# Performance work log

Measured on AMD Instinct MI355X. Metric: run time of the kernel, lower is better.

The kernel has to match this reference:

```python
import jax, jax.numpy as jnp
import numpy as np

BN_EPS = 1e-5
N_NODES = 100000
N_EDGES = 1600000
IN_DIM = 128
HID = 256   # 2 * out_dim
OUT_DIM = 128


def setup_inputs() -> dict:
    key = jax.random.key(0)
    ks = jax.random.split(key, 8)
    x = jax.random.normal(ks[0], (N_NODES, IN_DIM), dtype=jnp.float32)
    edge_index = jax.random.randint(ks[1], (2, N_EDGES), 0, N_NODES, dtype=jnp.int32)
    # GINConv learned eps (train_eps=True), init 0
    eps = jnp.zeros((), dtype=jnp.float32)
    # MLP: Linear(in, 2*out) -> BN -> ReLU -> Linear(2*out, out)
    s1 = 1.0 / np.sqrt(IN_DIM)
    s2 = 1.0 / np.sqrt(HID)
    W1 = jax.random.uniform(ks[2], (IN_DIM, HID), jnp.float32, -s1, s1)
    b1 = jax.random.uniform(ks[3], (HID,), jnp.float32, -s1, s1)
    g1 = jnp.ones((HID,), jnp.float32)
    beta1 = jnp.zeros((HID,), jnp.float32)
    W2 = jax.random.uniform(ks[4], (HID, OUT_DIM), jnp.float32, -s2, s2)
    b2 = jax.random.uniform(ks[5], (OUT_DIM,), jnp.float32, -s2, s2)
    # outer BatchNorm
    g2 = jnp.ones((OUT_DIM,), jnp.float32)
    beta2 = jnp.zeros((OUT_DIM,), jnp.float32)
    return {"x": x, "edge_index": edge_index, "eps": eps,
            "W1": W1, "b1": b1, "g1": g1, "beta1": beta1,
            "W2": W2, "b2": b2, "g2": g2, "beta2": beta2}


def _batchnorm(h, gamma, beta):
    # training-mode BatchNorm1d: batch mean, biased variance
    mu = jnp.mean(h, axis=0)
    var = jnp.mean(jnp.square(h - mu), axis=0)
    return (h - mu) * jax.lax.rsqrt(var + BN_EPS) * gamma + beta


def reference(x, edge_index, eps, W1, b1, g1, beta1, W2, b2, g2, beta2):
    src, dst = edge_index[0], edge_index[1]
    # sum-aggregation of neighbor features: scatter-add x[src] onto dst
    aggr = jax.ops.segment_sum(x[src], dst, num_segments=x.shape[0])  # [N, in_dim]
    h = (1.0 + eps) * x + aggr
    # MLP: Linear -> BN -> ReLU -> Linear
    h = h @ W1 + b1
    h = jax.nn.relu(_batchnorm(h, g1, beta1))
    h = h @ W2 + b2
    # outer BN + ReLU
    return jax.nn.relu(_batchnorm(h, g2, beta2))
```

## Files before the change

kernel.cpp:

```cpp
#include <hip/hip_runtime.h>
#include <hip/hip_bf16.h>

#define N_NODES 100000
#define N_EDGES 1600000
#define IN_DIM  128
#define HID     256
#define OUT_DIM 128
#define BN_EPS  1e-5f

typedef unsigned int u32;
typedef unsigned short u16;
typedef __attribute__((ext_vector_type(8))) short short8v;
typedef __attribute__((ext_vector_type(4))) float f32x4;

__device__ __forceinline__ float bf2f(u16 h) {
    return __uint_as_float(((u32)h) << 16);
}
__device__ __forceinline__ u16 f2bf(float f) {
    u32 u = __float_as_uint(f);
    u32 r = (u + 0x7fffu + ((u >> 16) & 1u)) >> 16;
    return (u16)r;
}
__device__ __forceinline__ u32 pack2(float a, float b) {
    return (u32)f2bf(a) | ((u32)f2bf(b) << 16);
}
__device__ __forceinline__ void gload16(const void* g, void* l) {
    __builtin_amdgcn_global_load_lds((const __attribute__((address_space(1))) u32*)g,
                                     (__attribute__((address_space(3))) u32*)l, 16, 0, 0);
}
#define MFMA(a,b,c) __builtin_amdgcn_mfma_f32_16x16x32_bf16(a, b, c, 0, 0, 0)

__global__ __launch_bounds__(256) void k_prep(const float* __restrict__ x,
                                              const int* __restrict__ ei,
                                              const float* __restrict__ W1,
                                              const float* __restrict__ W2,
                                              uint2* __restrict__ xb,
                                              int* __restrict__ head2,
                                              int2* __restrict__ nxt,
                                              char* __restrict__ w1t,
                                              char* __restrict__ w2t) {
    int t = blockIdx.x * 256 + threadIdx.x;
    {
        float4 v = ((const float4*)x)[t];
        uint2 p;
        p.x = pack2(v.x, v.y);
        p.y = pack2(v.z, v.w);
        xb[t] = p;
    }
    if (t < N_EDGES) {
        int dst = ei[N_EDGES + t];
        int src = ei[t];
        int old = atomicExch(&head2[dst * 2 + (t & 1)], t);
        nxt[t] = make_int2(old, src);
    }
    if (t < 8192) {
        u16 tmp[8];
        if (t < 4096) {
            int j = t >> 4, kc = t & 15;
            #pragma unroll
            for (int i = 0; i < 8; ++i) tmp[i] = f2bf(W1[(kc * 8 + i) * HID + j]);
            u32 off = ((u32)(j * 256 + kc * 16)) ^ (((u32)(j & 7)) << 4);
            uint4 q;
            q.x = (u32)tmp[0] | ((u32)tmp[1] << 16);
            q.y = (u32)tmp[2] | ((u32)tmp[3] << 16);
            q.z = (u32)tmp[4] | ((u32)tmp[5] << 16);
            q.w = (u32)tmp[6] | ((u32)tmp[7] << 16);
            *(uint4*)(w1t + off) = q;
        } else {
            int t2 = t - 4096;
            int j = t2 >> 5, kc = t2 & 31;
            #pragma unroll
            for (int i = 0; i < 8; ++i) tmp[i] = f2bf(W2[(kc * 8 + i) * OUT_DIM + j]);
            u32 off = ((u32)(j * 512 + kc * 16)) ^ (((u32)(j & 7)) << 4);
            uint4 q;
            q.x = (u32)tmp[0] | ((u32)tmp[1] << 16);
            q.y = (u32)tmp[2] | ((u32)tmp[3] << 16);
            q.z = (u32)tmp[4] | ((u32)tmp[5] << 16);
            q.w = (u32)tmp[6] | ((u32)tmp[7] << 16);
            *(uint4*)(w2t + off) = q;
        }
    }
}

__global__ __launch_bounds__(256) void k_aggregate(const uint4* __restrict__ xb4,
                                                   const int2* __restrict__ nxt,
                                                   const int* __restrict__ head2,
                                                   const float* __restrict__ epsp,
                                                   char* __restrict__ aggrb) {
    const int lane = threadIdx.x & 63;
    const int w = threadIdx.x >> 6;
    const int q = lane >> 4, l = lane & 15;
    const int nq = q >> 1, p = q & 1;
    const int node = blockIdx.x * 8 + w * 2 + nq;

    float a[8];
    #pragma unroll
    for (int i = 0; i < 8; ++i) a[i] = 0.f;

    if (p == 0) {
        float sc = 1.0f + epsp[0];
        uint4 v = xb4[node * 16 + l];
        a[0] = bf2f((u16)v.x) * sc;  a[1] = bf2f((u16)(v.x >> 16)) * sc;
        a[2] = bf2f((u16)v.y) * sc;  a[3] = bf2f((u16)(v.y >> 16)) * sc;
        a[4] = bf2f((u16)v.z) * sc;  a[5] = bf2f((u16)(v.z >> 16)) * sc;
        a[6] = bf2f((u16)v.w) * sc;  a[7] = bf2f((u16)(v.w >> 16)) * sc;
    }
    int e = head2[node * 2 + p];
    while (e >= 0) {
        int2 nv = nxt[e];
        e = nv.x;
        uint4 v = xb4[nv.y * 16 + l];
        a[0] += bf2f((u16)v.x);  a[1] += bf2f((u16)(v.x >> 16));
        a[2] += bf2f((u16)v.y);  a[3] += bf2f((u16)(v.y >> 16));
        a[4] += bf2f((u16)v.z);  a[5] += bf2f((u16)(v.z >> 16));
        a[6] += bf2f((u16)v.w);  a[7] += bf2f((u16)(v.w >> 16));
    }
    #pragma unroll
    for (int i = 0; i < 8; ++i) a[i] += __shfl_xor(a[i], 16);
    if (p == 0) {
        uint4 o;
        o.x = pack2(a[0], a[1]);
        o.y = pack2(a[2], a[3]);
        o.z = pack2(a[4], a[5]);
        o.w = pack2(a[6], a[7]);
        u32 b = ((u32)node * 256 + (u32)l * 16) ^ (((u32)(node & 7)) << 4);
        *(uint4*)(aggrb + b) = o;
    }
}

__global__ __launch_bounds__(512) void k_gemm1(const char* __restrict__ aggrb,
                                               const char* __restrict__ w1t,
                                               const float* __restrict__ b1,
                                               u16* __restrict__ h1t,
                                               float* __restrict__ gstats) {
    __shared__ u16 Als[160 * 128];
    __shared__ u16 Bls[256 * 128];
    __shared__ float slds[512];

    const int tid = threadIdx.x, lane = tid & 63, w = tid >> 6;
    const int wr = w >> 2, wc = w & 3;
    const int base = blockIdx.x * 160;

    slds[tid] = 0.f;

    char* lA = (char*)Als;
    char* lB = (char*)Bls;
    const char* ga = aggrb + (size_t)base * 256;
    #pragma unroll
    for (int i = 0; i < 5; ++i)
        gload16(ga + i * 8192 + w * 1024 + (lane << 4), lA + i * 8192 + w * 1024);
    #pragma unroll
    for (int i = 0; i < 8; ++i)
        gload16(w1t + i * 8192 + w * 1024 + (lane << 4), lB + i * 8192 + w * 1024);

    const int rA = lane & 15;
    const int q = lane >> 4;
    const int kb = q << 3;
    const u32 xsw = ((u32)(rA & 7)) << 4;
    int colv[4]; float bcol[4];
    #pragma unroll
    for (int n = 0; n < 4; ++n) { colv[n] = wc * 64 + n * 16 + rA; bcol[n] = b1[colv[n]]; }

    asm volatile("s_waitcnt vmcnt(0)" ::: "memory");
    __syncthreads();

    f32x4 acc[5][4];
    #pragma unroll
    for (int m = 0; m < 5; ++m)
        #pragma unroll
        for (int n = 0; n < 4; ++n) acc[m][n] = (f32x4){0.f, 0.f, 0.f, 0.f};

    #pragma unroll
    for (int ks = 0; ks < 4; ++ks) {
        const int kk2 = (ks * 32 + kb) * 2;
        short8v a[5], b[4];
        #pragma unroll
        for (int m = 0; m < 5; ++m) {
            u32 off = ((u32)((wr * 80 + m * 16 + rA) * 256 + kk2)) ^ xsw;
            a[m] = *(const short8v*)(lA + off);
        }
        #pragma unroll
        for (int n = 0; n < 4; ++n) {
            u32 off = ((u32)(colv[n] * 256 + kk2)) ^ xsw;
            b[n] = *(const short8v*)(lB + off);
        }
        #pragma unroll
        for (int m = 0; m < 5; ++m)
            #pragma unroll
            for (int n = 0; n < 4; ++n)
                acc[m][n] = MFMA(a[m], b[n], acc[m][n]);
    }

    const int Tb = blockIdx.x * 10 + wr * 5;
    float csum[4] = {0.f,0.f,0.f,0.f}, csq[4] = {0.f,0.f,0.f,0.f};
    #pragma unroll
    for (int m = 0; m < 5; ++m) {
        int T = Tb + m;
        #pragma unroll
        for (int n = 0; n < 4; ++n) {
            f32x4 d = acc[m][n];
            float v0 = d[0] + bcol[n], v1 = d[1] + bcol[n];
            float v2 = d[2] + bcol[n], v3 = d[3] + bcol[n];
            csum[n] += v0 + v1 + v2 + v3;
            csq[n]  += v0*v0 + v1*v1 + v2*v2 + v3*v3;
            uint2 p; p.x = pack2(v0, v1); p.y = pack2(v2, v3);
            *(uint2*)(h1t + (size_t)T * 4096 + colv[n] * 16 + q * 4) = p;
        }
    }
    #pragma unroll
    for (int n = 0; n < 4; ++n) {
        csum[n] += __shfl_xor(csum[n], 16); csum[n] += __shfl_xor(csum[n], 32);
        csq[n]  += __shfl_xor(csq[n], 16);  csq[n]  += __shfl_xor(csq[n], 32);
    }
    if (lane < 16) {
        #pragma unroll
        for (int n = 0; n < 4; ++n) {
            atomicAdd(&slds[colv[n]], csum[n]);
            atomicAdd(&slds[256 + colv[n]], csq[n]);
        }
    }
    __syncthreads();
    atomicAdd(&gstats[tid], slds[tid]);
}

__global__ __launch_bounds__(512) void k_gemm2(const uint4* __restrict__ h1t4,
                                               const char* __restrict__ w2t,
                                               const float* __restrict__ b2,
                                               const float* __restrict__ g1,
                                               const float* __restrict__ beta1,
                                               const float* __restrict__ gstats,
                                               u16* __restrict__ h2t,
                                               float* __restrict__ gstats2) {
    __shared__ u16 Als[160 * 128];
    __shared__ u16 Bls[128 * 256];
    __shared__ float a1s[256], b1s[256];
    __shared__ float slds[256];

    const int tid = threadIdx.x, lane = tid & 63, w = tid >> 6;
    const int wr = w >> 2, wc = w & 3;
    const int Tbase = blockIdx.x * 10;

    if (tid < 256) {
        float s = gstats[tid], sq = gstats[256 + tid];
        float mu = s * (1.0f / N_NODES);
        float var = sq * (1.0f / N_NODES) - mu * mu;
        float inv = rsqrtf(var + BN_EPS);
        float a = g1[tid] * inv;
        a1s[tid] = a;
        b1s[tid] = beta1[tid] - mu * a;
        slds[tid] = 0.f;
    }

    char* lA = (char*)Als;
    char* lB = (char*)Bls;
    #pragma unroll
    for (int i = 0; i < 8; ++i)
        gload16(w2t + i * 8192 + w * 1024 + (lane << 4), lB + i * 8192 + w * 1024);

    const int rA = lane & 15;
    const int q = lane >> 4;
    const int kb = q << 3;
    const u32 xsw = ((u32)(rA & 7)) << 4;
    int colv[2]; float bcol[2];
    #pragma unroll
    for (int n = 0; n < 2; ++n) { colv[n] = wc * 32 + n * 16 + rA; bcol[n] = b2[colv[n]]; }

    __syncthreads();

    f32x4 acc[5][2];
    #pragma unroll
    for (int m = 0; m < 5; ++m)
        #pragma unroll
        for (int n = 0; n < 2; ++n) acc[m][n] = (f32x4){0.f, 0.f, 0.f, 0.f};

    for (int kh = 0; kh < 2; ++kh) {
        #pragma unroll
        for (int i = 0; i < 5; ++i) {
            int id = i * 512 + tid;
            int kl = id & 127;
            int h16 = (id >> 7) & 1;
            int Tl = id >> 8;
            int kg = kh * 128 + kl;
            uint4 v = h1t4[(size_t)(Tbase + Tl) * 512 + kg * 2 + h16];
            float a = a1s[kg], b = b1s[kg];
            int r0 = Tl * 16 + h16 * 8;
            u16 hv[8] = {(u16)v.x, (u16)(v.x >> 16), (u16)v.y, (u16)(v.y >> 16),
                         (u16)v.z, (u16)(v.z >> 16), (u16)v.w, (u16)(v.w >> 16)};
            #pragma unroll
            for (int rr = 0; rr < 8; ++rr) {
                float f = fmaxf(bf2f(hv[rr]) * a + b, 0.f);
                int r = r0 + rr;
                u32 off = ((u32)(r * 256 + kl * 2)) ^ (((u32)(r & 7)) << 4);
                *(u16*)(lA + off) = f2bf(f);
            }
        }
        if (kh == 0) asm volatile("s_waitcnt vmcnt(0)" ::: "memory");
        __syncthreads();

        #pragma unroll
        for (int ks = 0; ks < 4; ++ks) {
            const int kk2 = (ks * 32 + kb) * 2;
            short8v a[5], b[2];
            #pragma unroll
            for (int n = 0; n < 2; ++n) {
                u32 off = ((u32)(colv[n] * 512 + kh * 256 + kk2)) ^ xsw;
                b[n] = *(const short8v*)(lB + off);
            }
            #pragma unroll
            for (int m = 0; m < 5; ++m) {
                u32 off = ((u32)((wr * 80 + m * 16 + rA) * 256 + kk2)) ^ xsw;
                a[m] = *(const short8v*)(lA + off);
            }
            #pragma unroll
            for (int m = 0; m < 5; ++m)
                #pragma unroll
                for (int n = 0; n < 2; ++n)
                    acc[m][n] = MFMA(a[m], b[n], acc[m][n]);
        }
        __syncthreads();
    }

    const int Tb = Tbase + wr * 5;
    float csum[2] = {0.f,0.f}, csq[2] = {0.f,0.f};
    #pragma unroll
    for (int m = 0; m < 5; ++m) {
        int T = Tb + m;
        #pragma unroll
        for (int n = 0; n < 2; ++n) {
            f32x4 d = acc[m][n];
            float v0 = d[0] + bcol[n], v1 = d[1] + bcol[n];
            float v2 = d[2] + bcol[n], v3 = d[3] + bcol[n];
            csum[n] += v0 + v1 + v2 + v3;
            csq[n]  += v0*v0 + v1*v1 + v2*v2 + v3*v3;
            uint2 p; p.x = pack2(v0, v1); p.y = pack2(v2, v3);
            *(uint2*)(h2t + (size_t)T * 2048 + colv[n] * 16 + q * 4) = p;
        }
    }
    #pragma unroll
    for (int n = 0; n < 2; ++n) {
        csum[n] += __shfl_xor(csum[n], 16); csum[n] += __shfl_xor(csum[n], 32);
        csq[n]  += __shfl_xor(csq[n], 16);  csq[n]  += __shfl_xor(csq[n], 32);
    }
    if (lane < 16) {
        #pragma unroll
        for (int n = 0; n < 2; ++n) {
            atomicAdd(&slds[colv[n]], csum[n]);
            atomicAdd(&slds[128 + colv[n]], csq[n]);
        }
    }
    __syncthreads();
    if (tid < 256) atomicAdd(&gstats2[tid], slds[tid]);
}

__global__ __launch_bounds__(256) void k_bn2(const uint4* __restrict__ h2t4,
                                             float* __restrict__ out,
                                             const float* __restrict__ gstats2,
                                             const float* __restrict__ g2,
                                             const float* __restrict__ beta2) {
    __shared__ float fl[32 * 128];
    __shared__ float a2s[128], b2s[128];
    const int tid = threadIdx.x;
    if (tid < 128) {
        float s = gstats2[tid], sq = gstats2[128 + tid];
        float mu = s * (1.0f / N_NODES);
        float var = sq * (1.0f / N_NODES) - mu * mu;
        float inv = rsqrtf(var + BN_EPS);
        float a = g2[tid] * inv;
        a2s[tid] = a;
        b2s[tid] = beta2[tid] - mu * a;
    }
    __syncthreads();
    const int Tbase = blockIdx.x * 2;
    #pragma unroll
    for (int i = 0; i < 2; ++i) {
        int id = i * 256 + tid;
        int kl = id & 127;
        int h16 = (id >> 7) & 1;
        int Tl = id >> 8;
        uint4 v = h2t4[(size_t)(Tbase + Tl) * 256 + kl * 2 + h16];
        float a = a2s[kl], b = b2s[kl];
        int r0 = Tl * 16 + h16 * 8;
        u16 hv[8] = {(u16)v.x, (u16)(v.x >> 16), (u16)v.y, (u16)(v.y >> 16),
                     (u16)v.z, (u16)(v.z >> 16), (u16)v.w, (u16)(v.w >> 16)};
        #pragma unroll
        for (int rr = 0; rr < 8; ++rr)
            fl[(r0 + rr) * 128 + kl] = fmaxf(bf2f(hv[rr]) * a + b, 0.f);
    }
    __syncthreads();
    #pragma unroll
    for (int i = 0; i < 4; ++i) {
        int id = i * 256 + tid;
        int row = id >> 5;
        int ch = id & 31;
        float4 vv = *(const float4*)&fl[row * 128 + ch * 4];
        ((float4*)out)[(size_t)(blockIdx.x * 32 + row) * 32 + ch] = vv;
    }
}

extern "C" void kernel_launch(void* const* d_in, const int* in_sizes, int n_in,
                              void* d_out, int out_size, void* d_ws, size_t ws_size,
                              hipStream_t stream) {
    const float* x     = (const float*)d_in[0];
    const int*   ei    = (const int*)d_in[1];
    const float* epsp  = (const float*)d_in[2];
    const float* W1    = (const float*)d_in[3];
    const float* b1    = (const float*)d_in[4];
    const float* g1    = (const float*)d_in[5];
    const float* beta1 = (const float*)d_in[6];
    const float* W2    = (const float*)d_in[7];
    const float* b2    = (const float*)d_in[8];
    const float* g2    = (const float*)d_in[9];
    const float* beta2 = (const float*)d_in[10];

    char* ws = (char*)d_ws;
    char*  aggrb   = ws;
    u16*   h2t     = (u16*)ws;
    u16*   h1t     = (u16*)(ws + 25600000);
    int2*  nxt     = (int2*)(ws + 25600000);
    int*   head2   = (int*)(ws + 38400000);
    uint2* xb      = (uint2*)(ws + 39200000);
    float* gstats  = (float*)(ws + 76800000);
    float* gstats2 = gstats + 512;
    char*  w1t     = ws + 76804096;
    char*  w2t     = ws + 76869632;
    float* out = (float*)d_out;

    hipMemsetAsync(head2, 0xFF, 800000, stream);
    hipMemsetAsync(gstats, 0, 768 * sizeof(float), stream);

    k_prep<<<12500, 256, 0, stream>>>(x, ei, W1, W2, xb, head2, nxt, w1t, w2t);
    k_aggregate<<<N_NODES / 8, 256, 0, stream>>>((const uint4*)xb, nxt, head2, epsp, aggrb);
    k_gemm1<<<625, 512, 0, stream>>>(aggrb, w1t, b1, h1t, gstats);
    k_gemm2<<<625, 512, 0, stream>>>((const uint4*)h1t, w2t, b2, g1, beta1, gstats, h2t, gstats2);
    k_bn2<<<3125, 256, 0, stream>>>((const uint4*)h2t, out, gstats2, g2, beta2);
}
```

Before: 257.0 us.

## Fuse neighbor aggregation into first GEMM and halve weight LDS footprint

```diff
diff --git a/kernel.cpp b/kernel.cpp
--- a/kernel.cpp
+++ b/kernel.cpp
@@ -38,7 +38,8 @@
                                               int* __restrict__ head2,
                                               int2* __restrict__ nxt,
                                               char* __restrict__ w1t,
-                                              char* __restrict__ w2t) {
+                                              char* __restrict__ w2t,
+                                              float* __restrict__ gstats) {
     int t = blockIdx.x * 256 + threadIdx.x;
     {
         float4 v = ((const float4*)x)[t];
@@ -53,6 +54,7 @@
         int old = atomicExch(&head2[dst * 2 + (t & 1)], t);
         nxt[t] = make_int2(old, src);
     }
+    if (t < 768) gstats[t] = 0.f;
     if (t < 8192) {
         u16 tmp[8];
         if (t < 4096) {
@@ -82,76 +84,66 @@
     }
 }
 
-__global__ __launch_bounds__(256) void k_aggregate(const uint4* __restrict__ xb4,
+__global__ __launch_bounds__(512, 4) void k_fused1(const uint4* __restrict__ xb4,
                                                    const int2* __restrict__ nxt,
                                                    const int* __restrict__ head2,
                                                    const float* __restrict__ epsp,
-                                                   char* __restrict__ aggrb) {
-    const int lane = threadIdx.x & 63;
-    const int w = threadIdx.x >> 6;
-    const int q = lane >> 4, l = lane & 15;
-    const int nq = q >> 1, p = q & 1;
-    const int node = blockIdx.x * 8 + w * 2 + nq;
-
-    float a[8];
-    #pragma unroll
-    for (int i = 0; i < 8; ++i) a[i] = 0.f;
-
-    if (p == 0) {
-        float sc = 1.0f + epsp[0];
-        uint4 v = xb4[node * 16 + l];
-        a[0] = bf2f((u16)v.x) * sc;  a[1] = bf2f((u16)(v.x >> 16)) * sc;
-        a[2] = bf2f((u16)v.y) * sc;  a[3] = bf2f((u16)(v.y >> 16)) * sc;
-        a[4] = bf2f((u16)v.z) * sc;  a[5] = bf2f((u16)(v.z >> 16)) * sc;
-        a[6] = bf2f((u16)v.w) * sc;  a[7] = bf2f((u16)(v.w >> 16)) * sc;
-    }
-    int e = head2[node * 2 + p];
-    while (e >= 0) {
-        int2 nv = nxt[e];
-        e = nv.x;
-        uint4 v = xb4[nv.y * 16 + l];
-        a[0] += bf2f((u16)v.x);  a[1] += bf2f((u16)(v.x >> 16));
-        a[2] += bf2f((u16)v.y);  a[3] += bf2f((u16)(v.y >> 16));
-        a[4] += bf2f((u16)v.z);  a[5] += bf2f((u16)(v.z >> 16));
-        a[6] += bf2f((u16)v.w);  a[7] += bf2f((u16)(v.w >> 16));
-    }
-    #pragma unroll
-    for (int i = 0; i < 8; ++i) a[i] += __shfl_xor(a[i], 16);
-    if (p == 0) {
-        uint4 o;
-        o.x = pack2(a[0], a[1]);
-        o.y = pack2(a[2], a[3]);
-        o.z = pack2(a[4], a[5]);
-        o.w = pack2(a[6], a[7]);
-        u32 b = ((u32)node * 256 + (u32)l * 16) ^ (((u32)(node & 7)) << 4);
-        *(uint4*)(aggrb + b) = o;
-    }
-}
-
-__global__ __launch_bounds__(512) void k_gemm1(const char* __restrict__ aggrb,
-                                               const char* __restrict__ w1t,
-                                               const float* __restrict__ b1,
-                                               u16* __restrict__ h1t,
-                                               float* __restrict__ gstats) {
+                                                   const char* __restrict__ w1t,
+                                                   const float* __restrict__ b1,
+                                                   u16* __restrict__ h1t,
+                                                   float* __restrict__ gstats) {
     __shared__ u16 Als[160 * 128];
-    __shared__ u16 Bls[256 * 128];
+    __shared__ u16 Bls[256 * 64];
     __shared__ float slds[512];
 
     const int tid = threadIdx.x, lane = tid & 63, w = tid >> 6;
     const int wr = w >> 2, wc = w & 3;
     const int base = blockIdx.x * 160;
-
-    slds[tid] = 0.f;
-
     char* lA = (char*)Als;
     char* lB = (char*)Bls;
-    const char* ga = aggrb + (size_t)base * 256;
-    #pragma unroll
-    for (int i = 0; i < 5; ++i)
-        gload16(ga + i * 8192 + w * 1024 + (lane << 4), lA + i * 8192 + w * 1024);
-    #pragma unroll
-    for (int i = 0; i < 8; ++i)
-        gload16(w1t + i * 8192 + w * 1024 + (lane << 4), lB + i * 8192 + w * 1024);
+
+    slds[tid] = 0.f;
+
+    {
+        const int q = lane >> 4, l = lane & 15;
+        const int nq = q >> 1, p = q & 1;
+        const float sc = 1.0f + epsp[0];
+        for (int r = 0; r < 10; ++r) {
+            const int row = r * 16 + w * 2 + nq;
+            const int node = base + row;
+            float a[8];
+            #pragma unroll
+            for (int i = 0; i < 8; ++i) a[i] = 0.f;
+            if (p == 0) {
+                uint4 v = xb4[node * 16 + l];
+                a[0] = bf2f((u16)v.x) * sc;  a[1] = bf2f((u16)(v.x >> 16)) * sc;
+                a[2] = bf2f((u16)v.y) * sc;  a[3] = bf2f((u16)(v.y >> 16)) * sc;
+                a[4] = bf2f((u16)v.z) * sc;  a[5] = bf2f((u16)(v.z >> 16)) * sc;
+                a[6] = bf2f((u16)v.w) * sc;  a[7] = bf2f((u16)(v.w >> 16)) * sc;
+            }
+            int e = head2[node * 2 + p];
+            while (e >= 0) {
+                int2 nv = nxt[e];
+                e = nv.x;
+                uint4 v = xb4[nv.y * 16 + l];
+                a[0] += bf2f((u16)v.x);  a[1] += bf2f((u16)(v.x >> 16));
+                a[2] += bf2f((u16)v.y);  a[3] += bf2f((u16)(v.y >> 16));
+                a[4] += bf2f((u16)v.z);  a[5] += bf2f((u16)(v.z >> 16));
+                a[6] += bf2f((u16)v.w);  a[7] += bf2f((u16)(v.w >> 16));
+            }
+            #pragma unroll
+            for (int i = 0; i < 8; ++i) a[i] += __shfl_xor(a[i], 16);
+            if (p == 0) {
+                uint4 o;
+                o.x = pack2(a[0], a[1]);
+                o.y = pack2(a[2], a[3]);
+                o.z = pack2(a[4], a[5]);
+                o.w = pack2(a[6], a[7]);
+                u32 b = ((u32)row * 256 + (u32)l * 16) ^ (((u32)(row & 7)) << 4);
+                *(uint4*)(lA + b) = o;
+            }
+        }
+    }
 
     const int rA = lane & 15;
     const int q = lane >> 4;
@@ -161,34 +153,44 @@
     #pragma unroll
     for (int n = 0; n < 4; ++n) { colv[n] = wc * 64 + n * 16 + rA; bcol[n] = b1[colv[n]]; }
 
-    asm volatile("s_waitcnt vmcnt(0)" ::: "memory");
-    __syncthreads();
-
     f32x4 acc[5][4];
     #pragma unroll
     for (int m = 0; m < 5; ++m)
         #pragma unroll
         for (int n = 0; n < 4; ++n) acc[m][n] = (f32x4){0.f, 0.f, 0.f, 0.f};
 
-    #pragma unroll
-    for (int ks = 0; ks < 4; ++ks) {
-        const int kk2 = (ks * 32 + kb) * 2;
-        short8v a[5], b[4];
-        #pragma unroll
-        for (int m = 0; m < 5; ++m) {
-            u32 off = ((u32)((wr * 80 + m * 16 + rA) * 256 + kk2)) ^ xsw;
-            a[m] = *(const short8v*)(lA + off);
-        }
-        #pragma unroll
-        for (int n = 0; n < 4; ++n) {
-            u32 off = ((u32)(colv[n] * 256 + kk2)) ^ xsw;
-            b[n] = *(const short8v*)(lB + off);
-        }
-        #pragma unroll
-        for (int m = 0; m < 5; ++m)
-            #pragma unroll
-            for (int n = 0; n < 4; ++n)
-                acc[m][n] = MFMA(a[m], b[n], acc[m][n]);
+    for (int kh = 0; kh < 2; ++kh) {
+        if (kh) __syncthreads();
+        #pragma unroll
+        for (int i = 0; i < 4; ++i) {
+            int idx = i * 512 + tid;
+            int j = idx >> 3, kc8 = idx & 7;
+            gload16(w1t + (u32)j * 256 + (u32)kh * 128 + (u32)kc8 * 16, lB + idx * 16);
+        }
+        asm volatile("s_waitcnt vmcnt(0)" ::: "memory");
+        __syncthreads();
+
+        #pragma unroll
+        for (int ksl = 0; ksl < 2; ++ksl) {
+            const int kk2A = (kh * 64 + ksl * 32 + kb) * 2;
+            const int kk2B = (ksl * 32 + kb) * 2;
+            short8v a[5], b[4];
+            #pragma unroll
+            for (int m = 0; m < 5; ++m) {
+                u32 off = ((u32)((wr * 80 + m * 16 + rA) * 256 + kk2A)) ^ xsw;
+                a[m] = *(const short8v*)(lA + off);
+            }
+            #pragma unroll
+            for (int n = 0; n < 4; ++n) {
+                u32 off = ((u32)(colv[n] * 128 + kk2B)) ^ xsw;
+                b[n] = *(const short8v*)(lB + off);
+            }
+            #pragma unroll
+            for (int m = 0; m < 5; ++m)
+                #pragma unroll
+                for (int n = 0; n < 4; ++n)
+                    acc[m][n] = MFMA(a[m], b[n], acc[m][n]);
+        }
     }
 
     const int Tb = blockIdx.x * 10 + wr * 5;
@@ -232,7 +234,7 @@
                                                u16* __restrict__ h2t,
                                                float* __restrict__ gstats2) {
     __shared__ u16 Als[160 * 128];
-    __shared__ u16 Bls[128 * 256];
+    __shared__ u16 Bls[128 * 128];
     __shared__ float a1s[256], b1s[256];
     __shared__ float slds[256];
 
@@ -253,9 +255,6 @@
 
     char* lA = (char*)Als;
     char* lB = (char*)Bls;
-    #pragma unroll
-    for (int i = 0; i < 8; ++i)
-        gload16(w2t + i * 8192 + w * 1024 + (lane << 4), lB + i * 8192 + w * 1024);
 
     const int rA = lane & 15;
     const int q = lane >> 4;
@@ -294,7 +293,14 @@
                 *(u16*)(lA + off) = f2bf(f);
             }
         }
-        if (kh == 0) asm volatile("s_waitcnt vmcnt(0)" ::: "memory");
+        #pragma unroll
+        for (int i = 0; i < 4; ++i) {
+            int idx = i * 512 + tid;
+            int j = idx >> 4, kc16 = idx & 15;
+            u32 src = (u32)j * 512 + (u32)kh * 256 + (u32)kc16 * 16;
+            gload16(w2t + src, lB + idx * 16);
+        }
+        asm volatile("s_waitcnt vmcnt(0)" ::: "memory");
         __syncthreads();
 
         #pragma unroll
@@ -303,7 +309,7 @@
             short8v a[5], b[2];
             #pragma unroll
             for (int n = 0; n < 2; ++n) {
-                u32 off = ((u32)(colv[n] * 512 + kh * 256 + kk2)) ^ xsw;
+                u32 off = ((u32)(colv[n] * 256 + kk2)) ^ xsw;
                 b[n] = *(const short8v*)(lB + off);
             }
             #pragma unroll
@@ -413,24 +419,21 @@
     const float* beta2 = (const float*)d_in[10];
 
     char* ws = (char*)d_ws;
-    char*  aggrb   = ws;
-    u16*   h2t     = (u16*)ws;
-    u16*   h1t     = (u16*)(ws + 25600000);
-    int2*  nxt     = (int2*)(ws + 25600000);
-    int*   head2   = (int*)(ws + 38400000);
-    uint2* xb      = (uint2*)(ws + 39200000);
-    float* gstats  = (float*)(ws + 76800000);
+    u16*   h1t     = (u16*)ws;
+    u16*   h2t     = (u16*)(ws + 51200000);
+    int2*  nxt     = (int2*)(ws + 51200000);
+    int*   head2   = (int*)(ws + 64000000);
+    uint2* xb      = (uint2*)(ws + 64800000);
+    float* gstats  = (float*)(ws + 90400000);
     float* gstats2 = gstats + 512;
-    char*  w1t     = ws + 76804096;
-    char*  w2t     = ws + 76869632;
+    char*  w1t     = ws + 90404096;
+    char*  w2t     = ws + 90469632;
     float* out = (float*)d_out;
 
     hipMemsetAsync(head2, 0xFF, 800000, stream);
-    hipMemsetAsync(gstats, 0, 768 * sizeof(float), stream);
-
-    k_prep<<<12500, 256, 0, stream>>>(x, ei, W1, W2, xb, head2, nxt, w1t, w2t);
-    k_aggregate<<<N_NODES / 8, 256, 0, stream>>>((const uint4*)xb, nxt, head2, epsp, aggrb);
-    k_gemm1<<<625, 512, 0, stream>>>(aggrb, w1t, b1, h1t, gstats);
+
+    k_prep<<<12500, 256, 0, stream>>>(x, ei, W1, W2, xb, head2, nxt, w1t, w2t, gstats);
+    k_fused1<<<625, 512, 0, stream>>>((const uint4*)xb, nxt, head2, epsp, w1t, b1, h1t, gstats);
     k_gemm2<<<625, 512, 0, stream>>>((const uint4*)h1t, w2t, b2, g1, beta1, gstats, h2t, gstats2);
     k_bn2<<<3125, 256, 0, stream>>>((const uint4*)h2t, out, gstats2, g2, beta2);
 }
```

Measured after the change: 352.7 us. +37.2%, slower.

## Split GEMM K loads in halves to shrink LDS and raise occupancy

Applied to the files above, without the earlier changes.

```diff
diff --git a/kernel.cpp b/kernel.cpp
--- a/kernel.cpp
+++ b/kernel.cpp
@@ -38,7 +38,8 @@
                                               int* __restrict__ head2,
                                               int2* __restrict__ nxt,
                                               char* __restrict__ w1t,
-                                              char* __restrict__ w2t) {
+                                              char* __restrict__ w2t,
+                                              float* __restrict__ gstats) {
     int t = blockIdx.x * 256 + threadIdx.x;
     {
         float4 v = ((const float4*)x)[t];
@@ -53,6 +54,7 @@
         int old = atomicExch(&head2[dst * 2 + (t & 1)], t);
         nxt[t] = make_int2(old, src);
     }
+    if (t < 768) gstats[t] = 0.f;
     if (t < 8192) {
         u16 tmp[8];
         if (t < 4096) {
@@ -128,30 +130,21 @@
     }
 }
 
-__global__ __launch_bounds__(512) void k_gemm1(const char* __restrict__ aggrb,
-                                               const char* __restrict__ w1t,
-                                               const float* __restrict__ b1,
-                                               u16* __restrict__ h1t,
-                                               float* __restrict__ gstats) {
-    __shared__ u16 Als[160 * 128];
-    __shared__ u16 Bls[256 * 128];
-    __shared__ float slds[512];
+__global__ __launch_bounds__(512, 6) void k_gemm1(const char* __restrict__ aggrb,
+                                                  const char* __restrict__ w1t,
+                                                  const float* __restrict__ b1,
+                                                  u16* __restrict__ h1t,
+                                                  float* __restrict__ gstats) {
+    __shared__ u16 Als[160 * 64];
+    __shared__ u16 Bls[256 * 64];
 
     const int tid = threadIdx.x, lane = tid & 63, w = tid >> 6;
     const int wr = w >> 2, wc = w & 3;
     const int base = blockIdx.x * 160;
 
-    slds[tid] = 0.f;
-
     char* lA = (char*)Als;
     char* lB = (char*)Bls;
     const char* ga = aggrb + (size_t)base * 256;
-    #pragma unroll
-    for (int i = 0; i < 5; ++i)
-        gload16(ga + i * 8192 + w * 1024 + (lane << 4), lA + i * 8192 + w * 1024);
-    #pragma unroll
-    for (int i = 0; i < 8; ++i)
-        gload16(w1t + i * 8192 + w * 1024 + (lane << 4), lB + i * 8192 + w * 1024);
 
     const int rA = lane & 15;
     const int q = lane >> 4;
@@ -161,34 +154,51 @@
     #pragma unroll
     for (int n = 0; n < 4; ++n) { colv[n] = wc * 64 + n * 16 + rA; bcol[n] = b1[colv[n]]; }
 
-    asm volatile("s_waitcnt vmcnt(0)" ::: "memory");
-    __syncthreads();
-
     f32x4 acc[5][4];
     #pragma unroll
     for (int m = 0; m < 5; ++m)
         #pragma unroll
         for (int n = 0; n < 4; ++n) acc[m][n] = (f32x4){0.f, 0.f, 0.f, 0.f};
 
-    #pragma unroll
-    for (int ks = 0; ks < 4; ++ks) {
-        const int kk2 = (ks * 32 + kb) * 2;
-        short8v a[5], b[4];
-        #pragma unroll
-        for (int m = 0; m < 5; ++m) {
-            u32 off = ((u32)((wr * 80 + m * 16 + rA) * 256 + kk2)) ^ xsw;
-            a[m] = *(const short8v*)(lA + off);
-        }
-        #pragma unroll
-        for (int n = 0; n < 4; ++n) {
-            u32 off = ((u32)(colv[n] * 256 + kk2)) ^ xsw;
-            b[n] = *(const short8v*)(lB + off);
-        }
-        #pragma unroll
-        for (int m = 0; m < 5; ++m)
-            #pragma unroll
-            for (int n = 0; n < 4; ++n)
-                acc[m][n] = MFMA(a[m], b[n], acc[m][n]);
+    for (int kh = 0; kh < 2; ++kh) {
+        if (kh) __syncthreads();
+        #pragma unroll
+        for (int i = 0; i < 3; ++i) {
+            int idx = i * 512 + tid;
+            if (idx < 1280) {
+                int r = idx >> 3, cc = idx & 7;
+                gload16(ga + r * 256 + kh * 128 + cc * 16, lA + idx * 16);
+            }
+        }
+        #pragma unroll
+        for (int i = 0; i < 4; ++i) {
+            int idx = i * 512 + tid;
+            int j = idx >> 3, kc8 = idx & 7;
+            gload16(w1t + (u32)j * 256 + (u32)kh * 128 + (u32)kc8 * 16, lB + idx * 16);
+        }
+        asm volatile("s_waitcnt vmcnt(0)" ::: "memory");
+        __syncthreads();
+
+        #pragma unroll
+        for (int ksl = 0; ksl < 2; ++ksl) {
+            const int kk2 = (ksl * 32 + kb) * 2;
+            short8v a[5], b[4];
+            #pragma unroll
+            for (int m = 0; m < 5; ++m) {
+                u32 off = ((u32)((wr * 80 + m * 16 + rA) * 128 + kk2)) ^ xsw;
+                a[m] = *(const short8v*)(lA + off);
+            }
+            #pragma unroll
+            for (int n = 0; n < 4; ++n) {
+                u32 off = ((u32)(colv[n] * 128 + kk2)) ^ xsw;
+                b[n] = *(const short8v*)(lB + off);
+            }
+            #pragma unroll
+            for (int m = 0; m < 5; ++m)
+                #pragma unroll
+                for (int n = 0; n < 4; ++n)
+                    acc[m][n] = MFMA(a[m], b[n], acc[m][n]);
+        }
     }
 
     const int Tb = blockIdx.x * 10 + wr * 5;
@@ -215,12 +225,10 @@
     if (lane < 16) {
         #pragma unroll
         for (int n = 0; n < 4; ++n) {
-            atomicAdd(&slds[colv[n]], csum[n]);
-            atomicAdd(&slds[256 + colv[n]], csq[n]);
-        }
-    }
-    __syncthreads();
-    atomicAdd(&gstats[tid], slds[tid]);
+            atomicAdd(&gstats[colv[n]], csum[n]);
+            atomicAdd(&gstats[256 + colv[n]], csq[n]);
+        }
+    }
 }
 
 __global__ __launch_bounds__(512) void k_gemm2(const uint4* __restrict__ h1t4,
@@ -232,7 +240,7 @@
                                                u16* __restrict__ h2t,
                                                float* __restrict__ gstats2) {
     __shared__ u16 Als[160 * 128];
-    __shared__ u16 Bls[128 * 256];
+    __shared__ u16 Bls[128 * 128];
     __shared__ float a1s[256], b1s[256];
     __shared__ float slds[256];
 
@@ -253,9 +261,6 @@
 
     char* lA = (char*)Als;
     char* lB = (char*)Bls;
-    #pragma unroll
-    for (int i = 0; i < 8; ++i)
-        gload16(w2t + i * 8192 + w * 1024 + (lane << 4), lB + i * 8192 + w * 1024);
 
     const int rA = lane & 15;
     const int q = lane >> 4;
@@ -274,6 +279,13 @@
         for (int n = 0; n < 2; ++n) acc[m][n] = (f32x4){0.f, 0.f, 0.f, 0.f};
 
     for (int kh = 0; kh < 2; ++kh) {
+        #pragma unroll
+        for (int i = 0; i < 4; ++i) {
+            int idx = i * 512 + tid;
+            int j = idx >> 4, kc16 = idx & 15;
+            u32 src = (u32)j * 512 + (u32)kh * 256 + (u32)kc16 * 16;
+            gload16(w2t + src, lB + idx * 16);
+        }
         #pragma unroll
         for (int i = 0; i < 5; ++i) {
             int id = i * 512 + tid;
@@ -294,7 +306,7 @@
                 *(u16*)(lA + off) = f2bf(f);
             }
         }
-        if (kh == 0) asm volatile("s_waitcnt vmcnt(0)" ::: "memory");
+        asm volatile("s_waitcnt vmcnt(0)" ::: "memory");
         __syncthreads();
 
         #pragma unroll
@@ -303,7 +315,7 @@
             short8v a[5], b[2];
             #pragma unroll
             for (int n = 0; n < 2; ++n) {
-                u32 off = ((u32)(colv[n] * 512 + kh * 256 + kk2)) ^ xsw;
+                u32 off = ((u32)(colv[n] * 256 + kk2)) ^ xsw;
                 b[n] = *(const short8v*)(lB + off);
             }
             #pragma unroll
@@ -426,9 +438,8 @@
     float* out = (float*)d_out;
 
     hipMemsetAsync(head2, 0xFF, 800000, stream);
-    hipMemsetAsync(gstats, 0, 768 * sizeof(float), stream);
-
-    k_prep<<<12500, 256, 0, stream>>>(x, ei, W1, W2, xb, head2, nxt, w1t, w2t);
+
+    k_prep<<<12500, 256, 0, stream>>>(x, ei, W1, W2, xb, head2, nxt, w1t, w2t, gstats);
     k_aggregate<<<N_NODES / 8, 256, 0, stream>>>((const uint4*)xb, nxt, head2, epsp, aggrb);
     k_gemm1<<<625, 512, 0, stream>>>(aggrb, w1t, b1, h1t, gstats);
     k_gemm2<<<625, 512, 0, stream>>>((const uint4*)h1t, w2t, b2, g1, beta1, gstats, h2t, gstats2);
```

Measured after the change: 351.3 us. 36.7% more time.
